# Optimization experiments

Measured on AMD Instinct MI355X. Metric: run time of the kernel, lower is better.

The kernel has to match this reference:

```python
import jax, jax.numpy as jnp
import numpy as np

B, F, H, K, E = 512, 1280, 2560, 8, 9  # batch, feat_dim, 2*feat_dim, branching, n_internal
# Tree: root=node 0 (expert 0); level-1 nodes 1..8 (experts 1..8); level-2 leaves 9..72.

def setup_inputs() -> dict:
    key = jax.random.key(0)
    k0, k1, k2, k3, k4 = jax.random.split(key, 5)
    x = jax.random.normal(k0, (B, F), dtype=jnp.float32)
    W1 = jax.random.normal(k1, (E, F, H), dtype=jnp.float32) / np.sqrt(F)
    b1 = jnp.zeros((E, H), dtype=jnp.float32)
    W2 = jax.random.normal(k2, (E, H, K), dtype=jnp.float32) / np.sqrt(H)
    b2 = jnp.zeros((E, K), dtype=jnp.float32)
    return {"x": x, "W1": W1, "b1": b1, "W2": W2, "b2": b2}

def reference(x, W1, b1, W2, b2):
    # Batched experts: Linear(F->H) -> ReLU -> Linear(H->K), softmax over children.
    h = jax.nn.relu(jnp.einsum('bf,efh->ebh', x, W1) + b1[:, None, :])  # [E,B,H]
    logits = jnp.einsum('ebh,ehk->ebk', h, W2) + b2[:, None, :]          # [E,B,K]
    probs = jax.nn.softmax(logits, axis=-1)                              # [E,B,K]
    # Path products root->node for every node (matches leaf_probs in torch code).
    p0 = jnp.ones((1, x.shape[0]), dtype=x.dtype)        # root: prob 1        [1,B]
    p1 = probs[0].T                                       # nodes 1..8          [K,B]
    # leaves 9..72: parent of node n is 1+(n-9)//K, child index (n-9)%K
    p2 = (p1[:, None, :] * jnp.transpose(probs[1:E], (0, 2, 1))).reshape(K * K, -1)  # [64,B]
    leaf_probs = jnp.concatenate([p0, p1, p2], axis=0).T  # [B, 73]
    return leaf_probs, logits
```

## Files before the change

kernel.cpp:

```cpp
#include <hip/hip_runtime.h>

#define TB 512
#define TF 1280
#define TH 2560
#define TK 8
#define TE 9
#define SLOT 8192
#define BUFSZ 16384

typedef unsigned short ushortT;
typedef unsigned long long u64;
typedef __attribute__((ext_vector_type(8))) short short8;
typedef __attribute__((ext_vector_type(4))) short short4v;
typedef __attribute__((ext_vector_type(4))) float floatx4;

__device__ __forceinline__ unsigned short f2bf(float f) {
  union { float f; unsigned u; } v; v.f = f;
  unsigned r = v.u + 0x7fffu + ((v.u >> 16) & 1u);
  return (unsigned short)(r >> 16);
}

__device__ __forceinline__ unsigned pk2(float a, float b) {
  union { float f; unsigned u; } ua, ub; ua.f = a; ub.f = b;
  unsigned ra = ua.u + 0x7fffu + ((ua.u >> 16) & 1u);
  unsigned rb = ub.u + 0x7fffu + ((ub.u >> 16) & 1u);
  return __builtin_amdgcn_perm(rb, ra, 0x07060302);
}

__device__ __forceinline__ void gl_lds16(const void* g, void* l) {
  __builtin_amdgcn_global_load_lds(
      (const __attribute__((address_space(1))) unsigned*)g,
      (__attribute__((address_space(3))) unsigned*)l, 16, 0, 0);
}

__device__ __forceinline__ int swz(int o) { return o ^ (((o >> 7) & 7) << 4); }

__global__ __launch_bounds__(256) void prep_all(
    const float* __restrict__ x, const float* __restrict__ W1,
    const float* __restrict__ W2,
    char* __restrict__ Apk, ushortT* __restrict__ W2t, char* __restrict__ W1p,
    float* __restrict__ lacc) {
  const int b = blockIdx.x;
  const int t = threadIdx.x;
  if (b < 7200) {
    __shared__ ushortT Ts[128 * 40];
    const int khalf = b & 1;
    const int kt = (b >> 1) % 20;
    const int nt = ((b >> 1) / 20) % 20;
    const int e = b / 800;
    const int kbase = kt * 64 + khalf * 32;
    const int nbase = nt * 128;
    const int kr = t >> 5, n4 = (t & 31) * 4;
#pragma unroll
    for (int kk = 0; kk < 4; ++kk) {
      const int k2 = kk * 8 + kr;
      floatx4 v = *(const floatx4*)(W1 + ((long)e * TF + kbase + k2) * TH + nbase + n4);
#pragma unroll
      for (int i = 0; i < 4; ++i) Ts[(n4 + i) * 40 + k2] = f2bf(v[i]);
    }
    __syncthreads();
    char* dstbase = W1p + (long)b * SLOT;
#pragma unroll
    for (int p = 0; p < 2; ++p) {
      const int op = (p * 256 + t) * 16;
      const int o = swz(op);
      const int r = o >> 6, k2c = (o & 63) >> 1;
      short8 v = *(const short8*)&Ts[r * 40 + k2c];
      *(short8*)(dstbase + op) = v;
    }
  } else if (b < 7520) {
    const int i = (b - 7200) * 256 + t;
    const int cc = i & 511, slot = i >> 9;
    const int khalf = slot & 1;
    const int kt = (slot >> 1) % 20;
    const int mt = slot / 40;
    const int op = cc * 16;
    const int o = swz(op);
    const int r = o >> 6, k2 = (o & 63) >> 1;
    const float* src = x + (long)(mt * 128 + r) * TF + kt * 64 + khalf * 32 + k2;
    floatx4 v0 = *(const floatx4*)(src);
    floatx4 v1 = *(const floatx4*)(src + 4);
    u64 q0 = (u64)pk2(v0.x, v0.y) | ((u64)pk2(v0.z, v0.w) << 32);
    u64 q1 = (u64)pk2(v1.x, v1.y) | ((u64)pk2(v1.z, v1.w) << 32);
    *(ulonglong2*)(Apk + (long)i * 16) = make_ulonglong2(q0, q1);
  } else if (b < 8240) {
    const int o = (b - 7520) * 256 + t;
    if (o < TE * TK * TH) {
      const int hcol = o % TH;
      const int rest = o / TH;
      const int n = rest & 7;
      const int e = rest >> 3;
      W2t[(long)(e * TK + n) * TH + hcol] = f2bf(W2[((long)e * TH + hcol) * TK + n]);
    }
  } else {
    const int i = ((b - 8240) * 256 + t) * 4;
    if (i < TE * TB * TK)
      *(floatx4*)(lacc + i) = (floatx4){0.f, 0.f, 0.f, 0.f};
  }
}

__global__ __launch_bounds__(256) void prepass(
    const float* __restrict__ x, const float* __restrict__ W2,
    u64* __restrict__ xq, ushortT* __restrict__ W2t) {
  const int i = blockIdx.x * 256 + threadIdx.x;
  if (i < 320 * 512) {
    const int kq = i >> 9, m = i & 511;
    floatx4 v = *(const floatx4*)(x + (long)m * TF + kq * 4);
    xq[i] = (u64)pk2(v.x, v.y) | ((u64)pk2(v.z, v.w) << 32);
  } else {
    const int o = i - 320 * 512;
    if (o < TE * TK * TH) {
      const int hcol = o % TH;
      const int rest = o / TH;
      const int n = rest & 7;
      const int e = rest >> 3;
      W2t[(long)(e * TK + n) * TH + hcol] = f2bf(W2[((long)e * TH + hcol) * TK + n]);
    }
  }
}

__global__ __launch_bounds__(256, 4) void gemm1_fused(
    const char* __restrict__ Apk, const char* __restrict__ Bpk,
    const float* __restrict__ b1, const ushortT* __restrict__ W2t,
    float* __restrict__ lacc) {
  __shared__ __align__(16) char lds[32768];
  const int t = threadIdx.x;
  const int lane = t & 63, w = t >> 6;
  const int wm = w >> 1, wn = w & 1;
  const int lm = lane & 15, lq = lane >> 4;
  const int bid0 = blockIdx.x;
  const int bs = (bid0 & 7) * 90 + (bid0 >> 3);
  const int mt = bs & 3;
  const int ct = bs >> 2;
  const int nt = ct % 20, e = ct / 20;

  const char* Ab = Apk + (long)mt * 40 * SLOT;
  const char* Bb = Bpk + (long)((e * 20 + nt) * 40) * SLOT;

  int oA[4], oB[4];
#pragma unroll
  for (int mi = 0; mi < 4; ++mi)
    oA[mi] = swz((wm * 64 + mi * 16 + lm) * 64 + lq * 16);
#pragma unroll
  for (int ni = 0; ni < 4; ++ni)
    oB[ni] = swz((wn * 64 + ni * 16 + lm) * 64 + lq * 16);

  auto STAGE = [&](int tile) {
    if (tile >= 40) return;
    char* dst = lds + (tile & 1) * BUFSZ + w * 1024;
    const char* sa = Ab + (long)tile * SLOT;
    const char* sb = Bb + (long)tile * SLOT;
    gl_lds16(sa + t * 16, dst);
    gl_lds16(sa + 4096 + t * 16, dst + 4096);
    gl_lds16(sb + t * 16, dst + 8192);
    gl_lds16(sb + 4096 + t * 16, dst + 12288);
  };

  floatx4 acc[4][4];
#pragma unroll
  for (int i = 0; i < 4; ++i)
#pragma unroll
    for (int j = 0; j < 4; ++j) acc[i][j] = (floatx4){0.f, 0.f, 0.f, 0.f};

  STAGE(0);
  asm volatile("s_waitcnt vmcnt(0)" ::: "memory");
  __builtin_amdgcn_s_barrier();

  for (int j = 0; j < 40; ++j) {
    const char* buf = lds + (j & 1) * BUFSZ;
    STAGE(j + 1);
    short8 af[4], bfr[4];
#pragma unroll
    for (int mi = 0; mi < 4; ++mi)
      af[mi] = *(const short8*)(buf + oA[mi]);
#pragma unroll
    for (int ni = 0; ni < 4; ++ni)
      bfr[ni] = *(const short8*)(buf + 8192 + oB[ni]);
    asm volatile("s_waitcnt lgkmcnt(0)" ::: "memory");
    __builtin_amdgcn_sched_barrier(0);
    __builtin_amdgcn_s_setprio(1);
#pragma unroll
    for (int mi = 0; mi < 4; ++mi)
#pragma unroll
      for (int ni = 0; ni < 4; ++ni)
        acc[mi][ni] = __builtin_amdgcn_mfma_f32_16x16x32_bf16(af[mi], bfr[ni], acc[mi][ni], 0, 0, 0);
    __builtin_amdgcn_s_setprio(0);
    asm volatile("s_waitcnt vmcnt(0)" ::: "memory");
    __builtin_amdgcn_s_barrier();
  }

  short8 bq[4];
  {
    const ushortT* wp = W2t + ((long)(e * TK + (lm < 8 ? lm : 0))) * TH
                        + nt * 128 + lq * 8;
#pragma unroll
    for (int kk = 0; kk < 4; ++kk) bq[kk] = *(const short8*)(wp + kk * 32);
    if (lm >= 8) {
#pragma unroll
      for (int kk = 0; kk < 4; ++kk) bq[kk] = (short8)0;
    }
  }

#pragma unroll
  for (int ni = 0; ni < 4; ++ni) {
    const int lcol = wn * 64 + ni * 16 + lm;
    const float bias = b1[e * TH + nt * 128 + lcol];
#pragma unroll
    for (int mi = 0; mi < 4; ++mi) {
      const int lr0 = wm * 64 + mi * 16 + lq * 4;
      floatx4 c = acc[mi][ni];
#pragma unroll
      for (int r = 0; r < 4; ++r) {
        float v = c[r] + bias;
        v = v > 0.f ? v : 0.f;
        const int lrow = lr0 + r;
        const int o = (lrow * 256 + lcol * 2) ^ ((lrow & 7) << 4);
        *(ushortT*)(lds + o) = f2bf(v);
      }
    }
  }
  __syncthreads();

  floatx4 acc2[2];
  acc2[0] = (floatx4){0.f, 0.f, 0.f, 0.f};
  acc2[1] = (floatx4){0.f, 0.f, 0.f, 0.f};
#pragma unroll
  for (int rt = 0; rt < 2; ++rt) {
    const int row = (w * 2 + rt) * 16 + lm;
    const int rowb = row * 256;
    const int sx = (row & 7) << 4;
#pragma unroll
    for (int kk = 0; kk < 4; ++kk) {
      short8 a = *(const short8*)(lds + ((rowb + kk * 64 + lq * 16) ^ sx));
      acc2[rt] = __builtin_amdgcn_mfma_f32_16x16x32_bf16(a, bq[kk], acc2[rt], 0, 0, 0);
    }
  }
  if (lm < 8) {
#pragma unroll
    for (int rt = 0; rt < 2; ++rt) {
      const int growb = mt * 128 + (w * 2 + rt) * 16 + lq * 4;
#pragma unroll
      for (int r = 0; r < 4; ++r)
        atomicAdd(&lacc[((long)e * TB + growb + r) * TK + lm], acc2[rt][r]);
    }
  }
}

__global__ __launch_bounds__(256) void finish(
    const float* __restrict__ lacc, const float* __restrict__ b2,
    float* __restrict__ out, float* __restrict__ logits_out) {
  const int b = blockIdx.x * 256 + threadIdx.x;
  if (b >= TB) return;
  float pr[TE][TK];
#pragma unroll
  for (int e = 0; e < TE; ++e) {
    float lg[TK];
    float mx = -1e30f;
#pragma unroll
    for (int k = 0; k < TK; ++k) {
      lg[k] = lacc[((long)e * TB + b) * TK + k] + b2[e * TK + k];
      logits_out[((long)e * TB + b) * TK + k] = lg[k];
      mx = fmaxf(mx, lg[k]);
    }
    float sm = 0.f;
#pragma unroll
    for (int k = 0; k < TK; ++k) { pr[e][k] = __expf(lg[k] - mx); sm += pr[e][k]; }
    const float inv = 1.f / sm;
#pragma unroll
    for (int k = 0; k < TK; ++k) pr[e][k] *= inv;
  }
  float* op = out + (long)b * 73;
  op[0] = 1.0f;
#pragma unroll
  for (int i = 0; i < 8; ++i) op[1 + i] = pr[0][i];
#pragma unroll
  for (int i = 0; i < 8; ++i)
#pragma unroll
    for (int j = 0; j < 8; ++j) op[9 + i * 8 + j] = pr[0][i] * pr[1 + i][j];
}

__global__ __launch_bounds__(256) void gemm1_fb(
    const float* __restrict__ x, const float* __restrict__ W1,
    const float* __restrict__ b1, ushortT* __restrict__ h) {
  __shared__ __align__(16) ushortT As[128 * 40];
  __shared__ __align__(16) ushortT Bs[128 * 40];
  const int t = threadIdx.x;
  const int tileN = blockIdx.x;
  const int e = tileN / 20;
  const int hbase = (tileN % 20) * 128;
  const int m0 = blockIdx.y * 128;
  const int lane = t & 63, w = t >> 6;
  const int wm = w & 1, wn = w >> 1;
  const int lm = lane & 15, lq = lane >> 4;
  const int lk = lq * 8;
  floatx4 acc[4][4];
#pragma unroll
  for (int i = 0; i < 4; ++i)
#pragma unroll
    for (int j = 0; j < 4; ++j) acc[i][j] = (floatx4){0.f, 0.f, 0.f, 0.f};
  const float* wp = W1 + (long)e * TF * TH + hbase;
  const int cA = (t & 7) * 4;
  const int mA = t >> 3;
  const int nB = t & 127;
  const int gB = t >> 7;
  for (int kt = 0; kt < TF / 32; ++kt) {
    const int k0 = kt * 32;
    if (kt) __syncthreads();
#pragma unroll
    for (int i = 0; i < 4; ++i) {
      const int m = mA + 32 * i;
      floatx4 v = *(const floatx4*)(x + (long)(m0 + m) * TF + k0 + cA);
      short4v s; s.x = f2bf(v.x); s.y = f2bf(v.y); s.z = f2bf(v.z); s.w = f2bf(v.w);
      *(short4v*)&As[m * 40 + cA] = s;
    }
    {
      const float* bp = wp + (long)k0 * TH + nB;
#pragma unroll
      for (int q = 0; q < 4; ++q) {
        const int k4 = gB * 16 + q * 4;
        float f0 = bp[(long)(k4 + 0) * TH];
        float f1 = bp[(long)(k4 + 1) * TH];
        float f2 = bp[(long)(k4 + 2) * TH];
        float f3 = bp[(long)(k4 + 3) * TH];
        short4v s; s.x = f2bf(f0); s.y = f2bf(f1); s.z = f2bf(f2); s.w = f2bf(f3);
        *(short4v*)&Bs[nB * 40 + k4] = s;
      }
    }
    __syncthreads();
    short8 af[4], bfr[4];
#pragma unroll
    for (int mg = 0; mg < 4; ++mg)
      af[mg] = *(const short8*)&As[(wm * 64 + mg * 16 + lm) * 40 + lk];
#pragma unroll
    for (int ng = 0; ng < 4; ++ng)
      bfr[ng] = *(const short8*)&Bs[(wn * 64 + ng * 16 + lm) * 40 + lk];
#pragma unroll
    for (int mg = 0; mg < 4; ++mg)
#pragma unroll
      for (int ng = 0; ng < 4; ++ng)
        acc[mg][ng] = __builtin_amdgcn_mfma_f32_16x16x32_bf16(af[mg], bfr[ng], acc[mg][ng], 0, 0, 0);
  }
#pragma unroll
  for (int mg = 0; mg < 4; ++mg) {
    const int row = m0 + wm * 64 + mg * 16 + lq * 4;
#pragma unroll
    for (int ng = 0; ng < 4; ++ng) {
      const int col = hbase + wn * 64 + ng * 16 + lm;
      const float bias = b1[e * TH + col];
      floatx4 c = acc[mg][ng];
#pragma unroll
      for (int r = 0; r < 4; ++r) {
        float v = c[r] + bias;
        v = v > 0.f ? v : 0.f;
        h[((long)e * TB + row + r) * TH + col] = f2bf(v);
      }
    }
  }
}

__global__ __launch_bounds__(512) void gemm2_softmax(
    const ushortT* __restrict__ h, const ushortT* __restrict__ W2t,
    const float* __restrict__ b2, float* __restrict__ logits_out,
    float* __restrict__ probs) {
  __shared__ float Ls[8][16][8];
  const int t = threadIdx.x;
  const int lane = t & 63, w = t >> 6;
  const int e = blockIdx.x >> 5;
  const int r0 = (blockIdx.x & 31) * 16;
  const int lm = lane & 15, lq = lane >> 4;

  const ushortT* hp = h + ((long)(e * TB + r0 + lm)) * TH + w * 320 + lq * 8;
  const int bn = lm < 8 ? lm : 7;
  const ushortT* wp = W2t + ((long)(e * TK + bn)) * TH + w * 320 + lq * 8;

  floatx4 acc = (floatx4){0.f, 0.f, 0.f, 0.f};
#pragma unroll
  for (int kt = 0; kt < 10; ++kt) {
    short8 a = *(const short8*)(hp + kt * 32);
    short8 b = *(const short8*)(wp + kt * 32);
    acc = __builtin_amdgcn_mfma_f32_16x16x32_bf16(a, b, acc, 0, 0, 0);
  }
  if (lm < 8) {
#pragma unroll
    for (int r = 0; r < 4; ++r) Ls[w][lq * 4 + r][lm] = acc[r];
  }
  __syncthreads();
  if (w == 0 && lm < 8) {
    const float bias = b2[e * TK + lm];
#pragma unroll
    for (int r = 0; r < 4; ++r) {
      const int row = lq * 4 + r;
      float v = Ls[0][row][lm] + Ls[1][row][lm] + Ls[2][row][lm] + Ls[3][row][lm]
              + Ls[4][row][lm] + Ls[5][row][lm] + Ls[6][row][lm] + Ls[7][row][lm]
              + bias;
      float mx = v;
      mx = fmaxf(mx, __shfl_xor(mx, 1, 64));
      mx = fmaxf(mx, __shfl_xor(mx, 2, 64));
      mx = fmaxf(mx, __shfl_xor(mx, 4, 64));
      float ex = __expf(v - mx);
      float sm = ex;
      sm += __shfl_xor(sm, 1, 64);
      sm += __shfl_xor(sm, 2, 64);
      sm += __shfl_xor(sm, 4, 64);
      const long idx = ((long)e * TB + r0 + row) * TK + lm;
      logits_out[idx] = v;
      probs[idx] = ex / sm;
    }
  }
}

__global__ __launch_bounds__(256) void leafk(const float* __restrict__ probs,
                                             float* __restrict__ out) {
  const int idx = blockIdx.x * 256 + threadIdx.x;
  if (idx >= TB * 73) return;
  const int b = idx / 73, c = idx % 73;
  float v;
  if (c == 0) {
    v = 1.0f;
  } else if (c < 9) {
    v = probs[(long)b * TK + (c - 1)];
  } else {
    const int i = (c - 9) >> 3, j = (c - 9) & 7;
    v = probs[(long)b * TK + i] * probs[((long)(1 + i) * TB + b) * TK + j];
  }
  out[idx] = v;
}

extern "C" void kernel_launch(void* const* d_in, const int* in_sizes, int n_in,
                              void* d_out, int out_size, void* d_ws, size_t ws_size,
                              hipStream_t stream) {
  const float* x  = (const float*)d_in[0];
  const float* W1 = (const float*)d_in[1];
  const float* b1 = (const float*)d_in[2];
  const float* W2 = (const float*)d_in[3];
  const float* b2 = (const float*)d_in[4];
  float* out = (float*)d_out;

  ushortT* h     = (ushortT*)d_ws;
  float*   lacc  = (float*)((char*)d_ws + 23592960);
  char*    Apk   = (char*)d_ws + 23740416;
  ushortT* W2t   = (ushortT*)((char*)d_ws + 25051136);
  char*    W1p   = (char*)d_ws + 25419776;
  const size_t NEED = 25419776 + 58982400;
  float* logits_out = out + TB * 73;

  if (ws_size >= NEED) {
    prep_all<<<8276, 256, 0, stream>>>(x, W1, W2, Apk, W2t, W1p, lacc);
    gemm1_fused<<<720, 256, 0, stream>>>(Apk, W1p, b1, W2t, lacc);
    finish<<<2, 256, 0, stream>>>(lacc, b2, out, logits_out);
  } else {
    prepass<<<1360, 256, 0, stream>>>(x, W2, (u64*)Apk, W2t);
    gemm1_fb<<<dim3(180, 4), 256, 0, stream>>>(x, W1, b1, h);
    gemm2_softmax<<<TE * 32, 512, 0, stream>>>(h, W2t, b2, logits_out, lacc);
    leafk<<<(TB * 73 + 255) / 256, 256, 0, stream>>>(lacc, out);
  }
}
```

Before: 228.5 us.

## Convert W1 to bf16 inside the GEMM instead of a separate repack pass

Removes the prep pass that transposed W1 into a packed, swizzled bf16 workspace. The fused GEMM now reads fp32 W1 directly into registers one tile ahead, converts it to bf16 and stores it into a double-buffered LDS region. The goal is to avoid writing and then re-reading the roughly 59 MB bf16 copy of W1. The cost is strided scalar global loads, reading fp32 instead of bf16 in the main loop (read traffic twice as large per tile), and extra register pressure and LDS stores in every iteration. Each of the 4 row tiles re-reads the same W1 columns in fp32.

Measured after the change: 232.7 us. Within noise of the previous version (+1.8%).

```diff
diff --git a/kernel.cpp b/kernel.cpp
--- a/kernel.cpp
+++ b/kernel.cpp
@@ -6,7 +6,6 @@
 #define TK 8
 #define TE 9
 #define SLOT 8192
-#define BUFSZ 16384
 
 typedef unsigned short ushortT;
 typedef unsigned long long u64;
@@ -36,40 +35,13 @@
 __device__ __forceinline__ int swz(int o) { return o ^ (((o >> 7) & 7) << 4); }
 
 __global__ __launch_bounds__(256) void prep_all(
-    const float* __restrict__ x, const float* __restrict__ W1,
-    const float* __restrict__ W2,
-    char* __restrict__ Apk, ushortT* __restrict__ W2t, char* __restrict__ W1p,
+    const float* __restrict__ x, const float* __restrict__ W2,
+    char* __restrict__ Apk, ushortT* __restrict__ W2t,
     float* __restrict__ lacc) {
   const int b = blockIdx.x;
   const int t = threadIdx.x;
-  if (b < 7200) {
-    __shared__ ushortT Ts[128 * 40];
-    const int khalf = b & 1;
-    const int kt = (b >> 1) % 20;
-    const int nt = ((b >> 1) / 20) % 20;
-    const int e = b / 800;
-    const int kbase = kt * 64 + khalf * 32;
-    const int nbase = nt * 128;
-    const int kr = t >> 5, n4 = (t & 31) * 4;
-#pragma unroll
-    for (int kk = 0; kk < 4; ++kk) {
-      const int k2 = kk * 8 + kr;
-      floatx4 v = *(const floatx4*)(W1 + ((long)e * TF + kbase + k2) * TH + nbase + n4);
-#pragma unroll
-      for (int i = 0; i < 4; ++i) Ts[(n4 + i) * 40 + k2] = f2bf(v[i]);
-    }
-    __syncthreads();
-    char* dstbase = W1p + (long)b * SLOT;
-#pragma unroll
-    for (int p = 0; p < 2; ++p) {
-      const int op = (p * 256 + t) * 16;
-      const int o = swz(op);
-      const int r = o >> 6, k2c = (o & 63) >> 1;
-      short8 v = *(const short8*)&Ts[r * 40 + k2c];
-      *(short8*)(dstbase + op) = v;
-    }
-  } else if (b < 7520) {
-    const int i = (b - 7200) * 256 + t;
+  if (b < 320) {
+    const int i = b * 256 + t;
     const int cc = i & 511, slot = i >> 9;
     const int khalf = slot & 1;
     const int kt = (slot >> 1) % 20;
@@ -83,17 +55,15 @@
     u64 q0 = (u64)pk2(v0.x, v0.y) | ((u64)pk2(v0.z, v0.w) << 32);
     u64 q1 = (u64)pk2(v1.x, v1.y) | ((u64)pk2(v1.z, v1.w) << 32);
     *(ulonglong2*)(Apk + (long)i * 16) = make_ulonglong2(q0, q1);
-  } else if (b < 8240) {
-    const int o = (b - 7520) * 256 + t;
-    if (o < TE * TK * TH) {
-      const int hcol = o % TH;
-      const int rest = o / TH;
-      const int n = rest & 7;
-      const int e = rest >> 3;
-      W2t[(long)(e * TK + n) * TH + hcol] = f2bf(W2[((long)e * TH + hcol) * TK + n]);
-    }
+  } else if (b < 1040) {
+    const int o = (b - 320) * 256 + t;
+    const int hcol = o % TH;
+    const int rest = o / TH;
+    const int n = rest & 7;
+    const int e = rest >> 3;
+    W2t[(long)(e * TK + n) * TH + hcol] = f2bf(W2[((long)e * TH + hcol) * TK + n]);
   } else {
-    const int i = ((b - 8240) * 256 + t) * 4;
+    const int i = ((b - 1040) * 256 + t) * 4;
     if (i < TE * TB * TK)
       *(floatx4*)(lacc + i) = (floatx4){0.f, 0.f, 0.f, 0.f};
   }
@@ -120,7 +90,7 @@
 }
 
 __global__ __launch_bounds__(256, 4) void gemm1_fused(
-    const char* __restrict__ Apk, const char* __restrict__ Bpk,
+    const char* __restrict__ Apk, const float* __restrict__ W1,
     const float* __restrict__ b1, const ushortT* __restrict__ W2t,
     float* __restrict__ lacc) {
   __shared__ __align__(16) char lds[32768];
@@ -135,7 +105,9 @@
   const int nt = ct % 20, e = ct / 20;
 
   const char* Ab = Apk + (long)mt * 40 * SLOT;
-  const char* Bb = Bpk + (long)((e * 20 + nt) * 40) * SLOT;
+  const int nB = t & 127;
+  const int gB = t >> 7;
+  const float* Wcol = W1 + (long)e * TF * TH + nt * 128 + nB;
 
   int oA[4], oB[4];
 #pragma unroll
@@ -145,37 +117,58 @@
   for (int ni = 0; ni < 4; ++ni)
     oB[ni] = swz((wn * 64 + ni * 16 + lm) * 64 + lq * 16);
 
-  auto STAGE = [&](int tile) {
+  auto STAGE_A = [&](int tile) {
     if (tile >= 40) return;
-    char* dst = lds + (tile & 1) * BUFSZ + w * 1024;
+    char* dst = lds + (tile & 1) * 8192 + w * 1024;
     const char* sa = Ab + (long)tile * SLOT;
-    const char* sb = Bb + (long)tile * SLOT;
     gl_lds16(sa + t * 16, dst);
     gl_lds16(sa + 4096 + t * 16, dst + 4096);
-    gl_lds16(sb + t * 16, dst + 8192);
-    gl_lds16(sb + 4096 + t * 16, dst + 12288);
   };
 
+  float bf32[16];
+  auto BLOAD = [&](int tile) {
+    if (tile >= 40) return;
+    const float* p = Wcol + (long)(tile * 32 + gB * 16) * TH;
+#pragma unroll
+    for (int q = 0; q < 16; ++q) bf32[q] = p[(long)q * TH];
+  };
+  auto BSTORE = [&](int tile) {
+    if (tile >= 40) return;
+    char* bb = lds + 16384 + (tile & 1) * 8192;
+#pragma unroll
+    for (int q = 0; q < 4; ++q) {
+      const int k4 = gB * 16 + q * 4;
+      u64 qw = (u64)pk2(bf32[q * 4 + 0], bf32[q * 4 + 1])
+             | ((u64)pk2(bf32[q * 4 + 2], bf32[q * 4 + 3]) << 32);
+      *(u64*)(bb + swz(nB * 64 + k4 * 2)) = qw;
+    }
+  };
+
   floatx4 acc[4][4];
 #pragma unroll
   for (int i = 0; i < 4; ++i)
 #pragma unroll
     for (int j = 0; j < 4; ++j) acc[i][j] = (floatx4){0.f, 0.f, 0.f, 0.f};
 
-  STAGE(0);
+  STAGE_A(0);
+  BLOAD(0);
   asm volatile("s_waitcnt vmcnt(0)" ::: "memory");
+  BSTORE(0);
+  asm volatile("s_waitcnt lgkmcnt(0)" ::: "memory");
   __builtin_amdgcn_s_barrier();
 
   for (int j = 0; j < 40; ++j) {
-    const char* buf = lds + (j & 1) * BUFSZ;
-    STAGE(j + 1);
+    const char* bufA = lds + (j & 1) * 8192;
+    const char* bufB = lds + 16384 + (j & 1) * 8192;
+    STAGE_A(j + 1);
+    BLOAD(j + 1);
     short8 af[4], bfr[4];
 #pragma unroll
     for (int mi = 0; mi < 4; ++mi)
-      af[mi] = *(const short8*)(buf + oA[mi]);
+      af[mi] = *(const short8*)(bufA + oA[mi]);
 #pragma unroll
     for (int ni = 0; ni < 4; ++ni)
-      bfr[ni] = *(const short8*)(buf + 8192 + oB[ni]);
+      bfr[ni] = *(const short8*)(bufB + oB[ni]);
     asm volatile("s_waitcnt lgkmcnt(0)" ::: "memory");
     __builtin_amdgcn_sched_barrier(0);
     __builtin_amdgcn_s_setprio(1);
@@ -186,6 +179,8 @@
         acc[mi][ni] = __builtin_amdgcn_mfma_f32_16x16x32_bf16(af[mi], bfr[ni], acc[mi][ni], 0, 0, 0);
     __builtin_amdgcn_s_setprio(0);
     asm volatile("s_waitcnt vmcnt(0)" ::: "memory");
+    BSTORE(j + 1);
+    asm volatile("s_waitcnt lgkmcnt(0)" ::: "memory");
     __builtin_amdgcn_s_barrier();
   }
 
@@ -301,8 +296,8 @@
   const float* wp = W1 + (long)e * TF * TH + hbase;
   const int cA = (t & 7) * 4;
   const int mA = t >> 3;
-  const int nB = t & 127;
-  const int gB = t >> 7;
+  const int nBf = t & 127;
+  const int gBf = t >> 7;
   for (int kt = 0; kt < TF / 32; ++kt) {
     const int k0 = kt * 32;
     if (kt) __syncthreads();
@@ -314,16 +309,16 @@
       *(short4v*)&As[m * 40 + cA] = s;
     }
     {
-      const float* bp = wp + (long)k0 * TH + nB;
+      const float* bp = wp + (long)k0 * TH + nBf;
 #pragma unroll
       for (int q = 0; q < 4; ++q) {
-        const int k4 = gB * 16 + q * 4;
+        const int k4 = gBf * 16 + q * 4;
         float f0 = bp[(long)(k4 + 0) * TH];
         float f1 = bp[(long)(k4 + 1) * TH];
         float f2 = bp[(long)(k4 + 2) * TH];
         float f3 = bp[(long)(k4 + 3) * TH];
         short4v s; s.x = f2bf(f0); s.y = f2bf(f1); s.z = f2bf(f2); s.w = f2bf(f3);
-        *(short4v*)&Bs[nB * 40 + k4] = s;
+        *(short4v*)&Bs[nBf * 40 + k4] = s;
       }
     }
     __syncthreads();
@@ -440,13 +435,12 @@
   float*   lacc  = (float*)((char*)d_ws + 23592960);
   char*    Apk   = (char*)d_ws + 23740416;
   ushortT* W2t   = (ushortT*)((char*)d_ws + 25051136);
-  char*    W1p   = (char*)d_ws + 25419776;
-  const size_t NEED = 25419776 + 58982400;
+  const size_t NEED = 25419776;
   float* logits_out = out + TB * 73;
 
   if (ws_size >= NEED) {
-    prep_all<<<8276, 256, 0, stream>>>(x, W1, W2, Apk, W2t, W1p, lacc);
-    gemm1_fused<<<720, 256, 0, stream>>>(Apk, W1p, b1, W2t, lacc);
+    prep_all<<<1076, 256, 0, stream>>>(x, W2, Apk, W2t, lacc);
+    gemm1_fused<<<720, 256, 0, stream>>>(Apk, W1, b1, W2t, lacc);
     finish<<<2, 256, 0, stream>>>(lacc, b2, out, logits_out);
   } else {
     prepass<<<1360, 256, 0, stream>>>(x, W2, (u64*)Apk, W2t);
```
